# Optimization experiments

Measured on AMD Instinct MI355X. Metric: run time of the kernel, lower is better.

## Reference

```python
import jax, jax.numpy as jnp
import numpy as np

N, IN, H, OUT, E = 4096, 128, 128, 2, 131072


def _hgnn(x, G, W, b):
    # HGNNConv (Feng et al.): X' = G @ (X W + b), G dense normalized [N,N]
    return G @ (x @ W + b)


def _mha(xin, Wqkv, bqkv, Wo, bo, nh):
    # torch.nn.MultiheadAttention, input (L, B, E), self-attention, eval mode
    L, B, Emb = xin.shape
    hd = Emb // nh
    qkv = xin @ Wqkv.T + bqkv                       # [L,B,3E]
    q, k, v = jnp.split(qkv, 3, axis=-1)
    def sh(t):
        return t.reshape(L, B, nh, hd).transpose(1, 2, 0, 3)  # [B,nh,L,hd]
    q, k, v = sh(q), sh(k), sh(v)
    att = jax.nn.softmax(jnp.einsum('bnld,bnmd->bnlm', q, k) / jnp.sqrt(jnp.float32(hd)), axis=-1)
    o = jnp.einsum('bnlm,bnmd->bnld', att, v).transpose(2, 0, 1, 3).reshape(L, B, Emb)
    return o @ Wo.T + bo


def setup_inputs() -> dict:
    key = jax.random.key(0)
    ks = jax.random.split(key, 40)
    d = {}
    d['x'] = jax.random.normal(ks[0], (N, IN), jnp.float32)
    # dense normalized hypergraph propagation matrices (rand, scaled ~1/N so rows sum ~1)
    d['hg_1hop'] = jax.random.uniform(ks[1], (N, N), jnp.float32) * (2.0 / N)
    d['hg_3hop'] = jax.random.uniform(ks[2], (N, N), jnp.float32) * (2.0 / N)
    d['edge_indices'] = jax.random.randint(ks[3], (2, E), 0, N).astype(jnp.int32)
    d['new_idb'] = jax.random.permutation(ks[4], N).astype(jnp.int32)
    d['lam'] = jax.random.uniform(ks[5], (1,), jnp.float32)
    d['beta'] = jnp.asarray(0.3, jnp.float32)
    i = 6
    def w(shape, s):
        nonlocal i
        out = jax.random.normal(ks[i], shape, jnp.float32) * s
        i += 1
        return out
    sw = 1.0 / np.sqrt(H)
    d['W1'] = w((IN, H), 1.0 / np.sqrt(IN)); d['b1'] = w((H,), 0.01)
    for nm in ['W2', 'W3', 'W1h', 'W3h', 'W2m', 'W3m']:
        d[nm] = w((H, H), sw); d['b' + nm[1:]] = w((H,), 0.01)
    for tag in ['mix', 'fus']:
        d['Wqkv_' + tag] = w((3 * H, H), sw); d['bqkv_' + tag] = w((3 * H,), 0.01)
        d['Wo_' + tag] = w((H, H), sw); d['bo_' + tag] = w((H,), 0.01)
    d['Wc'] = w((2 * H, OUT), 1.0 / np.sqrt(2 * H)); d['bc'] = w((OUT,), 0.01)
    return d


def reference(x, hg_1hop, hg_3hop, edge_indices, new_idb, lam, beta,
              W1, b1, W2, b2, W3, b3, W1h, b1h, W3h, b3h, W2m, b2m, W3m, b3m,
              Wqkv_mix, bqkv_mix, Wo_mix, bo_mix,
              Wqkv_fus, bqkv_fus, Wo_fus, bo_fus, Wc, bc):
    # eval mode: dropout = identity
    h1 = jax.nn.relu(_hgnn(x, hg_1hop, W1, b1))
    h2 = jax.nn.relu(_hgnn(h1, hg_1hop, W2, b2) + h1)
    h3_c1 = jax.nn.relu(_hgnn(h2, hg_1hop, W3, b3) + h2)

    # shuffle_hypergraph: permute nodes of the dense incidence-derived matrix
    hg1_b = hg_1hop[new_idb][:, new_idb]
    hg3_b = hg_3hop[new_idb][:, new_idb]
    l = lam[0]
    # mixup_hidden: manifold mixup of propagated features with permuted graph/features
    h1_mix_1hop = l * _hgnn(h1, hg_1hop, W1h, b1h) + (1.0 - l) * _hgnn(h1[new_idb], hg1_b, W1h, b1h)
    h1_mix_3hop = l * _hgnn(h1, hg_3hop, W3h, b3h) + (1.0 - l) * _hgnn(h1[new_idb], hg3_b, W3h, b3h)

    h1_stack = jnp.stack([h1_mix_1hop, h1_mix_3hop], axis=0)     # [2,N,H]
    h1_mix = _mha(h1_stack, Wqkv_mix, bqkv_mix, Wo_mix, bo_mix, 2).mean(axis=0)
    h2_mix = jax.nn.relu(_hgnn(h1_mix, hg_1hop, W2m, b2m) + h1_mix)
    h3_c2 = jax.nn.relu(_hgnn(h2_mix, hg_1hop, W3m, b3m) + h2_mix) * beta

    h3_stack = jnp.stack([h3_c1, h3_c2], axis=0)                 # [2,N,H]
    h3 = _mha(h3_stack, Wqkv_fus, bqkv_fus, Wo_fus, bo_fus, 4).mean(axis=0)

    edge_emb = jnp.concatenate([h3[edge_indices[0]], h3[edge_indices[1]]], axis=1)  # [E,2H]
    edge_pred = edge_emb @ Wc + bc
    return edge_pred, h3
```

## Files before the change

kernel.cpp:

```cpp
#include <hip/hip_runtime.h>
#include <math.h>

typedef unsigned short u16;
typedef short s8v __attribute__((ext_vector_type(8)));
typedef float f4v __attribute__((ext_vector_type(4)));

__device__ inline float b2f(u16 u) {
    union { unsigned int i; float f; } v; v.i = ((unsigned int)u) << 16; return v.f;
}
__device__ inline u16 f2b(float f) {
    unsigned int x = __float_as_uint(f);
    return (u16)((x + 0x7fffu + ((x >> 16) & 1u)) >> 16);
}
__device__ inline float ldf(const void* p, size_t i, int f32) {
    return f32 ? ((const float*)p)[i] : b2f(((const u16*)p)[i]);
}
__device__ inline s8v load8(const void* p, size_t idx, int f32) {
    if (f32) {
        const float* f = (const float*)p + idx;
        float4 a = *(const float4*)(f);
        float4 b = *(const float4*)(f + 4);
        s8v r;
        r[0] = (short)f2b(a.x); r[1] = (short)f2b(a.y);
        r[2] = (short)f2b(a.z); r[3] = (short)f2b(a.w);
        r[4] = (short)f2b(b.x); r[5] = (short)f2b(b.y);
        r[6] = (short)f2b(b.z); r[7] = (short)f2b(b.w);
        return r;
    }
    return *(const s8v*)((const u16*)p + idx);
}

__global__ void detect_kernel(const u16* __restrict__ hg, int* __restrict__ flag) {
    int lane = threadIdx.x;
    bool ok = true;
    for (int i = 0; i < 32; ++i) {
        float v = b2f(hg[lane * 32 + i]);
        ok = ok && (fabsf(v) <= 1e-3f);
    }
    unsigned long long m = __ballot(ok);
    if (lane == 0) *flag = (m == ~0ull) ? 0 : 1;
}

__global__ __launch_bounds__(512) void big_gemm(const void* __restrict__ G,
                                                const u16* __restrict__ Zt,
                                                float* __restrict__ part,
                                                int kChunkLen,
                                                const int* __restrict__ dflag) {
    __shared__ u16 At[128 * 72];
    __shared__ u16 Bt[128 * 72];
    const int f32 = *dflag;
    const int tid = threadIdx.x;
    const int rowBase = blockIdx.x * 128;
    const int kChunk = blockIdx.y * kChunkLen;
    const int w = tid >> 6, lane = tid & 63;
    const int wm = w & 1, wn = w >> 1;
    const int l15 = lane & 15, quad = lane >> 4;
    const int nIter = kChunkLen >> 6;

    const int r0 = tid >> 3, kb0 = tid & 7;
    const int r1 = 64 + (tid >> 3), kb1 = tid & 7;

    f4v acc[4][2] = {};

    for (int it = 0; it < nIter; ++it) {
        const int kBase = kChunk + it * 64;
        s8v ga0 = load8(G, (size_t)(rowBase + r0) * 4096 + kBase + kb0 * 8, f32);
        s8v gb0 = *(const s8v*)(Zt + (size_t)r0 * 4096 + kBase + kb0 * 8);
        s8v ga1 = load8(G, (size_t)(rowBase + r1) * 4096 + kBase + kb1 * 8, f32);
        s8v gb1 = *(const s8v*)(Zt + (size_t)r1 * 4096 + kBase + kb1 * 8);
        __syncthreads();
        *(s8v*)(At + r0 * 72 + kb0 * 8) = ga0;
        *(s8v*)(Bt + r0 * 72 + kb0 * 8) = gb0;
        *(s8v*)(At + r1 * 72 + kb1 * 8) = ga1;
        *(s8v*)(Bt + r1 * 72 + kb1 * 8) = gb1;
        __syncthreads();
#pragma unroll
        for (int ks = 0; ks < 2; ++ks) {
            s8v a[4], b[2];
            const int kq = ks * 4 + quad;
#pragma unroll
            for (int mi = 0; mi < 4; ++mi)
                a[mi] = *(const s8v*)(At + (wm * 64 + mi * 16 + l15) * 72 + kq * 8);
#pragma unroll
            for (int ni = 0; ni < 2; ++ni)
                b[ni] = *(const s8v*)(Bt + (wn * 32 + ni * 16 + l15) * 72 + kq * 8);
#pragma unroll
            for (int mi = 0; mi < 4; ++mi)
#pragma unroll
                for (int ni = 0; ni < 2; ++ni)
                    acc[mi][ni] = __builtin_amdgcn_mfma_f32_16x16x32_bf16(
                        a[mi], b[ni], acc[mi][ni], 0, 0, 0);
        }
    }
    float* pbase = part + (size_t)blockIdx.y * 4096 * 128;
#pragma unroll
    for (int mi = 0; mi < 4; ++mi)
#pragma unroll
        for (int ni = 0; ni < 2; ++ni) {
            int row = rowBase + wm * 64 + mi * 16 + quad * 4;
            int col = wn * 32 + ni * 16 + l15;
#pragma unroll
            for (int r = 0; r < 4; ++r)
                pbase[(size_t)(row + r) * 128 + col] = acc[mi][ni][r];
        }
}

__global__ __launch_bounds__(256) void reduce_epi(const float* __restrict__ part,
                                                  const u16* __restrict__ res,
                                                  const void* __restrict__ betap,
                                                  u16* __restrict__ out, int mode,
                                                  int S, const int* __restrict__ dflag) {
    int i = (blockIdx.x * 256 + threadIdx.x) * 4;
    f4v t = {};
    for (int s = 0; s < S; ++s)
        t += *(const f4v*)(part + (size_t)s * 524288 + i);
    float bscale = (mode == 2) ? ldf(betap, 0, *dflag) : 1.0f;
    u16 o[4];
#pragma unroll
    for (int j = 0; j < 4; ++j) {
        float v = t[j];
        if (mode == 1 || mode == 2) v += b2f(res[i + j]);
        if (mode <= 2) v = fmaxf(v, 0.0f);
        if (mode == 2) v *= bscale;
        o[j] = f2b(v);
    }
    *(ushort4*)(out + i) = make_ushort4(o[0], o[1], o[2], o[3]);
}

__global__ __launch_bounds__(256) void feat_gemm(const void* __restrict__ A,
                                                 const void* __restrict__ W,
                                                 const void* __restrict__ bias,
                                                 void* __restrict__ out,
                                                 u16* __restrict__ mirror,
                                                 size_t outOfs,
                                                 int M, int NcTotal, int wLayout,
                                                 int outMode, int aRaw, int outRaw,
                                                 const int* __restrict__ dflag) {
    __shared__ char smem[52224];
    u16* Wt = (u16*)smem;
    u16* At = (u16*)(smem + 34816);
    u16* Tt = (u16*)smem;
    const int f32 = *dflag;
    const int aF32 = aRaw & f32;
    const int tid = threadIdx.x;
    const int rowBase = blockIdx.x * 64;
    const int colBase = blockIdx.y * 128;

    if (wLayout == 1) {
#pragma unroll
        for (int i = 0; i < 8; ++i) {
            int c = i * 256 + tid;
            int n = c >> 4, kb = c & 15;
            s8v v = load8(W, (size_t)(colBase + n) * 128 + kb * 8, f32);
            *(s8v*)(Wt + n * 136 + kb * 8) = v;
        }
    } else {
#pragma unroll
        for (int i = 0; i < 64; ++i) {
            int idx = i * 256 + tid;
            int k = idx >> 7, n = idx & 127;
            Wt[n * 136 + k] = f2b(ldf(W, (size_t)k * NcTotal + colBase + n, f32));
        }
    }
#pragma unroll
    for (int i = 0; i < 4; ++i) {
        int c = i * 256 + tid;
        int r = c >> 4, kb = c & 15;
        s8v v = load8(A, (size_t)(rowBase + r) * 128 + kb * 8, aF32);
        *(s8v*)(At + r * 136 + kb * 8) = v;
    }
    __syncthreads();

    const int w = tid >> 6, lane = tid & 63, l15 = lane & 15, quad = lane >> 4;
    f4v acc[8] = {};
#pragma unroll
    for (int ks = 0; ks < 4; ++ks) {
        int k = ks * 32 + quad * 8;
        s8v a = *(const s8v*)(At + (w * 16 + l15) * 136 + k);
#pragma unroll
        for (int ni = 0; ni < 8; ++ni) {
            s8v b = *(const s8v*)(Wt + (ni * 16 + l15) * 136 + k);
            acc[ni] = __builtin_amdgcn_mfma_f32_16x16x32_bf16(a, b, acc[ni], 0, 0, 0);
        }
    }

    if (outMode == 0) {
#pragma unroll
        for (int ni = 0; ni < 8; ++ni) {
            int n = colBase + ni * 16 + l15;
            float bv = ldf(bias, n, f32);
#pragma unroll
            for (int r = 0; r < 4; ++r) {
                int row = rowBase + w * 16 + quad * 4 + r;
                size_t idx = (size_t)row * NcTotal + n;
                float v = acc[ni][r] + bv;
                u16 vb = f2b(v);
                if (outRaw && f32) ((float*)out)[outOfs + idx] = v;
                else               ((u16*)out)[outOfs + idx] = vb;
                if (mirror) mirror[idx] = vb;
            }
        }
    } else {
        __syncthreads();
#pragma unroll
        for (int ni = 0; ni < 8; ++ni) {
            int n = ni * 16 + l15;
            float bv = ldf(bias, colBase + n, f32);
#pragma unroll
            for (int r = 0; r < 4; ++r)
                Tt[n * 72 + (w * 16 + quad * 4 + r)] = f2b(acc[ni][r] + bv);
        }
        __syncthreads();
#pragma unroll
        for (int i = 0; i < 4; ++i) {
            int c = i * 256 + tid;
            int h = c >> 3, nb = c & 7;
            s8v v = *(const s8v*)(Tt + h * 72 + nb * 8);
            *(s8v*)((u16*)out + (size_t)(colBase + h) * M + rowBase + nb * 8) = v;
        }
    }
}

__global__ __launch_bounds__(256) void mix_kernel(const u16* __restrict__ Ph1,
                                                  const u16* __restrict__ Ph3,
                                                  const int* __restrict__ perm,
                                                  const void* __restrict__ lamp,
                                                  u16* __restrict__ xin,
                                                  const int* __restrict__ dflag) {
    int i = blockIdx.x * 256 + threadIdx.x;
    int n = i >> 7, h = i & 127;
    float l = ldf(lamp, 0, *dflag);
    int pn = perm[n];
    float a = l * b2f(Ph1[i]) + (1.0f - l) * b2f(Ph1[(size_t)pn * 128 + h]);
    float b = l * b2f(Ph3[i]) + (1.0f - l) * b2f(Ph3[(size_t)pn * 128 + h]);
    xin[i] = f2b(a);
    xin[524288 + i] = f2b(b);
}

__global__ __launch_bounds__(256) void attn_kernel(const u16* __restrict__ qkv,
                                                   u16* __restrict__ obar, int nh) {
    int wid = threadIdx.x >> 6, lane = threadIdx.x & 63;
    int n = blockIdx.x * 4 + wid;
    const u16* r0 = qkv + (size_t)n * 384;
    const u16* r1 = qkv + (size_t)(4096 + n) * 384;
    int hd = 128 / nh;
    float scale = 1.0f / sqrtf((float)hd);
    float ov[2];
#pragma unroll
    for (int e = 0; e < 2; ++e) {
        int h = e * 64 + lane;
        float q0 = b2f(r0[h]),       q1 = b2f(r1[h]);
        float k0 = b2f(r0[128 + h]), k1 = b2f(r1[128 + h]);
        float v0 = b2f(r0[256 + h]), v1 = b2f(r1[256 + h]);
        float s00 = q0 * k0, s01 = q0 * k1, s10 = q1 * k0, s11 = q1 * k1;
        for (int off = hd >> 1; off; off >>= 1) {
            s00 += __shfl_xor(s00, off);
            s01 += __shfl_xor(s01, off);
            s10 += __shfl_xor(s10, off);
            s11 += __shfl_xor(s11, off);
        }
        s00 *= scale; s01 *= scale; s10 *= scale; s11 *= scale;
        float m0 = fmaxf(s00, s01), m1 = fmaxf(s10, s11);
        float e00 = expf(s00 - m0), e01 = expf(s01 - m0);
        float e10 = expf(s10 - m1), e11 = expf(s11 - m1);
        float a00 = e00 / (e00 + e01), a01 = e01 / (e00 + e01);
        float a10 = e10 / (e10 + e11), a11 = e11 / (e10 + e11);
        float o0 = a00 * v0 + a01 * v1;
        float o1 = a10 * v0 + a11 * v1;
        ov[e] = 0.5f * (o0 + o1);
    }
    obar[(size_t)n * 128 + lane] = f2b(ov[0]);
    obar[(size_t)n * 128 + 64 + lane] = f2b(ov[1]);
}

__global__ __launch_bounds__(256) void edge_kernel(const u16* __restrict__ h3,
                                                   const int* __restrict__ eidx,
                                                   const void* __restrict__ Wc,
                                                   const void* __restrict__ bc,
                                                   void* __restrict__ out,
                                                   const int* __restrict__ dflag) {
    __shared__ float w0[256], w1[256];
    const int f32 = *dflag;
    int t = threadIdx.x;
    w0[t] = ldf(Wc, (size_t)t * 2, f32);
    w1[t] = ldf(Wc, (size_t)t * 2 + 1, f32);
    __syncthreads();
    int e = blockIdx.x * 256 + t;
    float a0 = ldf(bc, 0, f32), a1 = ldf(bc, 1, f32);
#pragma unroll
    for (int p = 0; p < 2; ++p) {
        int node = eidx[p * 131072 + e];
        const s8v* row = (const s8v*)(h3 + (size_t)node * 128);
#pragma unroll
        for (int cch = 0; cch < 16; ++cch) {
            s8v d = row[cch];
#pragma unroll
            for (int j = 0; j < 8; ++j) {
                float f = b2f((u16)d[j]);
                int k = p * 128 + cch * 8 + j;
                a0 += f * w0[k];
                a1 += f * w1[k];
            }
        }
    }
    if (f32) {
        ((float*)out)[(size_t)e * 2] = a0;
        ((float*)out)[(size_t)e * 2 + 1] = a1;
    } else {
        ((u16*)out)[(size_t)e * 2] = f2b(a0);
        ((u16*)out)[(size_t)e * 2 + 1] = f2b(a1);
    }
}

extern "C" void kernel_launch(void* const* d_in, const int* in_sizes, int n_in,
                              void* d_out, int out_size, void* d_ws, size_t ws_size,
                              hipStream_t stream) {
    const void* x    = d_in[0];
    const void* G1   = d_in[1];
    const void* G3   = d_in[2];
    const int* eidx = (const int*)d_in[3];
    const int* perm = (const int*)d_in[4];
    const void* lam  = d_in[5];
    const void* beta = d_in[6];
    const void* W1 = d_in[7],  *b1 = d_in[8];
    const void* W2 = d_in[9],  *b2 = d_in[10];
    const void* W3 = d_in[11], *b3 = d_in[12];
    const void* W1h = d_in[13], *b1h = d_in[14];
    const void* W3h = d_in[15], *b3h = d_in[16];
    const void* W2m = d_in[17], *b2m = d_in[18];
    const void* W3m = d_in[19], *b3m = d_in[20];
    const void* Wqkv_mix = d_in[21], *bqkv_mix = d_in[22];
    const void* Wo_mix   = d_in[23], *bo_mix   = d_in[24];
    const void* Wqkv_fus = d_in[25], *bqkv_fus = d_in[26];
    const void* Wo_fus   = d_in[27], *bo_fus   = d_in[28];
    const void* Wc = d_in[29], *bc = d_in[30];

    const size_t MB = 1ull << 20;
    char* base = (char*)d_ws;
    u16* Zt    = (u16*)(base + 0 * MB);
    u16* h1    = (u16*)(base + 1 * MB);
    u16* h2    = (u16*)(base + 2 * MB);
    u16* h3c1  = (u16*)(base + 3 * MB);
    u16* h1mix = (u16*)(base + 4 * MB);
    u16* h2mix = (u16*)(base + 5 * MB);
    u16* h3c2  = (u16*)(base + 6 * MB);
    u16* Ph1   = (u16*)(base + 7 * MB);
    u16* Ph3   = (u16*)(base + 8 * MB);
    int* dflag = (int*)(base + 9 * MB);
    char* pool = base + 9 * MB + 65536;
    size_t poolBytes = (ws_size > 9 * MB + 65536) ? ws_size - 9 * MB - 65536 : 0;
    int S = (poolBytes >= 16 * MB) ? 8 : (poolBytes >= 8 * MB) ? 4
          : (poolBytes >= 4 * MB) ? 2 : 1;
    int kLen = 4096 / S;
    float* part = (float*)pool;
    u16* xin  = (u16*)pool;
    u16* qkv  = (u16*)(pool + 2 * MB);
    u16* obar = (u16*)pool;

    auto feat = [&](const void* A, const void* W, const void* b, void* o,
                    u16* mir, size_t ofs, int M, int Nc, int wl, int om,
                    int aRaw, int oRaw) {
        feat_gemm<<<dim3(M / 64, Nc / 128), 256, 0, stream>>>(
            A, W, b, o, mir, ofs, M, Nc, wl, om, aRaw, oRaw, dflag);
    };
    auto big = [&](const void* Gm) {
        big_gemm<<<dim3(32, S), 512, 0, stream>>>(Gm, Zt, part, kLen, dflag);
    };
    auto epi = [&](const u16* res, u16* o, int mode) {
        reduce_epi<<<512, 256, 0, stream>>>(part, res, beta, o, mode, S, dflag);
    };

    detect_kernel<<<1, 64, 0, stream>>>((const u16*)G1, dflag);

    feat(x, W1, b1, Zt, nullptr, 0, 4096, 128, 0, 1, 1, 0);  big(G1);  epi(nullptr, h1, 0);
    feat(h1, W2, b2, Zt, nullptr, 0, 4096, 128, 0, 1, 0, 0); big(G1);  epi(h1, h2, 1);
    feat(h1, W1h, b1h, Zt, nullptr, 0, 4096, 128, 0, 1, 0, 0); big(G1); epi(nullptr, Ph1, 3);
    feat(h1, W3h, b3h, Zt, nullptr, 0, 4096, 128, 0, 1, 0, 0); big(G3); epi(nullptr, Ph3, 3);
    feat(h2, W3, b3, Zt, nullptr, 0, 4096, 128, 0, 1, 0, 0); big(G1);  epi(h2, h3c1, 1);
    mix_kernel<<<2048, 256, 0, stream>>>(Ph1, Ph3, perm, lam, xin, dflag);
    feat(xin, Wqkv_mix, bqkv_mix, qkv, nullptr, 0, 8192, 384, 1, 0, 0, 0);
    attn_kernel<<<1024, 256, 0, stream>>>(qkv, obar, 2);
    feat(obar, Wo_mix, bo_mix, h1mix, nullptr, 0, 4096, 128, 1, 0, 0, 0);
    feat(h1mix, W2m, b2m, Zt, nullptr, 0, 4096, 128, 0, 1, 0, 0); big(G1); epi(h1mix, h2mix, 1);
    feat(h2mix, W3m, b3m, Zt, nullptr, 0, 4096, 128, 0, 1, 0, 0); big(G1); epi(h2mix, h3c2, 2);
    feat(h3c1, Wqkv_fus, bqkv_fus, qkv, nullptr, 0, 4096, 384, 1, 0, 0, 0);
    feat(h3c2, Wqkv_fus, bqkv_fus, qkv + (size_t)4096 * 384, nullptr, 0, 4096, 384, 1, 0, 0, 0);
    attn_kernel<<<1024, 256, 0, stream>>>(qkv, obar, 4);
    feat(obar, Wo_fus, bo_fus, d_out, Zt, (size_t)131072 * 2, 4096, 128, 1, 0, 0, 1);
    edge_kernel<<<512, 256, 0, stream>>>(Zt, eidx, Wc, bc, d_out, dflag);
}
```

Baseline: 643.4 us.

## Fuse whole forward into one cooperative persistent kernel with grid syncs

Replaces about thirty separate kernel launches with a single cooperative kernel of 256 blocks that runs every stage and separates them with grid.sync. It also converts G1 to bf16 once when the input is fp32, and runs independent feature and propagation GEMMs back to back within a phase (three big GEMMs into separate partial buffers), which removes launch gaps and some serialization. The cost is that the stages are tied to a fixed 256-block grid that may underuse the GPU, the kernel carries register and occupancy pressure, it needs 102 MB of workspace, and it falls back to the old path if the cooperative launch fails.

```diff
diff --git a/kernel.cpp b/kernel.cpp
--- a/kernel.cpp
+++ b/kernel.cpp
@@ -1,5 +1,8 @@
 #include <hip/hip_runtime.h>
+#include <hip/hip_cooperative_groups.h>
 #include <math.h>
+
+namespace cg = cooperative_groups;
 
 typedef unsigned short u16;
 typedef short s8v __attribute__((ext_vector_type(8)));
@@ -28,6 +31,318 @@
         return r;
     }
     return *(const s8v*)((const u16*)p + idx);
+}
+
+struct MP {
+    const void *x, *G1, *G3; const int *eidx, *perm; const void *lam, *beta;
+    const void *W1,*b1,*W2,*b2,*W3,*b3,*W1h,*b1h,*W3h,*b3h,*W2m,*b2m,*W3m,*b3m;
+    const void *Wqkv_mix,*bqkv_mix,*Wo_mix,*bo_mix,*Wqkv_fus,*bqkv_fus,*Wo_fus,*bo_fus,*Wc,*bc;
+    void* out;
+    u16 *G1b,*Zt0,*Zt1,*Zt2,*Zt3,*h1,*h2,*h3c1,*h1mix,*h2mix,*h3c2,*Ph1,*Ph3,*xin,*qkv,*obar,*mir;
+    float *part0,*part1,*part2;
+};
+
+__device__ void feat_stage(char* smemc, int bid, int tid, int f32,
+                           const void* A, int aF32,
+                           const void* W, const void* bias, int wLayout,
+                           int M, int Nc, int outMode, void* outp, u16* mir, int outF32) {
+    u16* Wt = (u16*)smemc;
+    u16* At = (u16*)(smemc + 34816);
+    const int w = tid >> 6, lane = tid & 63, l15 = lane & 15, quad = lane >> 4;
+    const int nSl = M >> 4;
+    for (int cb = 0; cb < Nc; cb += 128) {
+        __syncthreads();
+        if (wLayout == 1) {
+            for (int c = tid; c < 2048; c += 512) {
+                int n = c >> 4, kb = c & 15;
+                *(s8v*)(Wt + n * 136 + kb * 8) = load8(W, (size_t)(cb + n) * 128 + kb * 8, f32);
+            }
+        } else {
+            for (int idx = tid; idx < 16384; idx += 512) {
+                int k = idx >> 7, n = idx & 127;
+                Wt[n * 136 + k] = f2b(ldf(W, (size_t)k * Nc + cb + n, f32));
+            }
+        }
+        __syncthreads();
+        for (int sl = bid; sl < nSl; sl += 256) {
+            if (tid < 256) {
+                int r = tid >> 4, kb = tid & 15;
+                *(s8v*)(At + r * 136 + kb * 8) = load8(A, (size_t)(sl * 16 + r) * 128 + kb * 8, aF32);
+            }
+            __syncthreads();
+            f4v acc = {};
+#pragma unroll
+            for (int ks = 0; ks < 4; ++ks) {
+                s8v a = *(const s8v*)(At + l15 * 136 + ks * 32 + quad * 8);
+                s8v b = *(const s8v*)(Wt + (w * 16 + l15) * 136 + ks * 32 + quad * 8);
+                acc = __builtin_amdgcn_mfma_f32_16x16x32_bf16(a, b, acc, 0, 0, 0);
+            }
+            int col = cb + w * 16 + l15;
+            float bv = ldf(bias, col, f32);
+            if (outMode == 1) {
+                ushort4 o4;
+                o4.x = f2b(acc[0] + bv); o4.y = f2b(acc[1] + bv);
+                o4.z = f2b(acc[2] + bv); o4.w = f2b(acc[3] + bv);
+                *(ushort4*)((u16*)outp + (size_t)col * M + sl * 16 + quad * 4) = o4;
+            } else if (outMode == 0) {
+#pragma unroll
+                for (int r = 0; r < 4; ++r) {
+                    int row = sl * 16 + quad * 4 + r;
+                    ((u16*)outp)[(size_t)row * Nc + col] = f2b(acc[r] + bv);
+                }
+            } else {
+#pragma unroll
+                for (int r = 0; r < 4; ++r) {
+                    int row = sl * 16 + quad * 4 + r;
+                    float v = acc[r] + bv;
+                    u16 vb = f2b(v);
+                    mir[(size_t)row * 128 + col] = vb;
+                    if (outF32) ((float*)outp)[262144 + (size_t)row * 128 + col] = v;
+                    else        ((u16*)outp)[262144 + (size_t)row * 128 + col] = vb;
+                }
+            }
+            __syncthreads();
+        }
+    }
+}
+
+__device__ void big_stage(char* smemc, int tid, int id, const void* G, int gF32,
+                          const u16* Zt, float* part) {
+    u16* At = (u16*)smemc;
+    u16* Bt = (u16*)(smemc + 18432);
+    const int rowBase = (id & 31) * 128;
+    const int kChunk = (id >> 5) * 512;
+    const int w = tid >> 6, lane = tid & 63;
+    const int wm = w & 1, wn = w >> 1;
+    const int l15 = lane & 15, quad = lane >> 4;
+    const int r0 = tid >> 3, kb = tid & 7, r1 = 64 + (tid >> 3);
+    f4v acc[4][2] = {};
+    for (int it = 0; it < 8; ++it) {
+        const int kBase = kChunk + it * 64;
+        s8v ga0 = load8(G, (size_t)(rowBase + r0) * 4096 + kBase + kb * 8, gF32);
+        s8v gb0 = *(const s8v*)(Zt + (size_t)r0 * 4096 + kBase + kb * 8);
+        s8v ga1 = load8(G, (size_t)(rowBase + r1) * 4096 + kBase + kb * 8, gF32);
+        s8v gb1 = *(const s8v*)(Zt + (size_t)r1 * 4096 + kBase + kb * 8);
+        __syncthreads();
+        *(s8v*)(At + r0 * 72 + kb * 8) = ga0;
+        *(s8v*)(Bt + r0 * 72 + kb * 8) = gb0;
+        *(s8v*)(At + r1 * 72 + kb * 8) = ga1;
+        *(s8v*)(Bt + r1 * 72 + kb * 8) = gb1;
+        __syncthreads();
+#pragma unroll
+        for (int ks = 0; ks < 2; ++ks) {
+            s8v a[4], b[2];
+            const int kq = ks * 4 + quad;
+#pragma unroll
+            for (int mi = 0; mi < 4; ++mi)
+                a[mi] = *(const s8v*)(At + (wm * 64 + mi * 16 + l15) * 72 + kq * 8);
+#pragma unroll
+            for (int ni = 0; ni < 2; ++ni)
+                b[ni] = *(const s8v*)(Bt + (wn * 32 + ni * 16 + l15) * 72 + kq * 8);
+#pragma unroll
+            for (int mi = 0; mi < 4; ++mi)
+#pragma unroll
+                for (int ni = 0; ni < 2; ++ni)
+                    acc[mi][ni] = __builtin_amdgcn_mfma_f32_16x16x32_bf16(
+                        a[mi], b[ni], acc[mi][ni], 0, 0, 0);
+        }
+    }
+    float* pbase = part + (size_t)(id >> 5) * 524288;
+#pragma unroll
+    for (int mi = 0; mi < 4; ++mi)
+#pragma unroll
+        for (int ni = 0; ni < 2; ++ni) {
+            int row = rowBase + wm * 64 + mi * 16 + quad * 4;
+            int col = wn * 32 + ni * 16 + l15;
+#pragma unroll
+            for (int r = 0; r < 4; ++r)
+                pbase[(size_t)(row + r) * 128 + col] = acc[mi][ni][r];
+        }
+}
+
+__device__ void epi_one(int gid, const float* part, const u16* res, u16* outb,
+                        int mode, float bscale) {
+    int i = gid * 4;
+    f4v t = {};
+#pragma unroll
+    for (int s = 0; s < 8; ++s)
+        t += *(const f4v*)(part + (size_t)s * 524288 + i);
+    u16 o[4];
+#pragma unroll
+    for (int j = 0; j < 4; ++j) {
+        float v = t[j];
+        if (mode == 1 || mode == 2) v += b2f(res[i + j]);
+        if (mode <= 2) v = fmaxf(v, 0.0f);
+        if (mode == 2) v *= bscale;
+        o[j] = f2b(v);
+    }
+    *(ushort4*)(outb + i) = make_ushort4(o[0], o[1], o[2], o[3]);
+}
+
+__device__ void mix_stage(int gid, const u16* Ph1, const u16* Ph3,
+                          const int* perm, float l, u16* xin) {
+    for (int i = gid; i < 524288; i += 131072) {
+        int n = i >> 7, h = i & 127;
+        int pn = perm[n];
+        float a = l * b2f(Ph1[i]) + (1.0f - l) * b2f(Ph1[(size_t)pn * 128 + h]);
+        float b = l * b2f(Ph3[i]) + (1.0f - l) * b2f(Ph3[(size_t)pn * 128 + h]);
+        xin[i] = f2b(a);
+        xin[524288 + i] = f2b(b);
+    }
+}
+
+__device__ void attn_stage(int bid, int tid, const u16* qkv, u16* obar, int nh) {
+    int w = tid >> 6, lane = tid & 63;
+    int hd = 128 / nh;
+    float scale = 1.0f / sqrtf((float)hd);
+    for (int n = bid * 8 + w; n < 4096; n += 2048) {
+        const u16* r0 = qkv + (size_t)n * 384;
+        const u16* r1 = qkv + (size_t)(4096 + n) * 384;
+        float ov[2];
+#pragma unroll
+        for (int e = 0; e < 2; ++e) {
+            int h = e * 64 + lane;
+            float q0 = b2f(r0[h]),       q1 = b2f(r1[h]);
+            float k0 = b2f(r0[128 + h]), k1 = b2f(r1[128 + h]);
+            float v0 = b2f(r0[256 + h]), v1 = b2f(r1[256 + h]);
+            float s00 = q0 * k0, s01 = q0 * k1, s10 = q1 * k0, s11 = q1 * k1;
+            for (int off = hd >> 1; off; off >>= 1) {
+                s00 += __shfl_xor(s00, off);
+                s01 += __shfl_xor(s01, off);
+                s10 += __shfl_xor(s10, off);
+                s11 += __shfl_xor(s11, off);
+            }
+            s00 *= scale; s01 *= scale; s10 *= scale; s11 *= scale;
+            float m0 = fmaxf(s00, s01), m1 = fmaxf(s10, s11);
+            float e00 = expf(s00 - m0), e01 = expf(s01 - m0);
+            float e10 = expf(s10 - m1), e11 = expf(s11 - m1);
+            float a00 = e00 / (e00 + e01), a01 = e01 / (e00 + e01);
+            float a10 = e10 / (e10 + e11), a11 = e11 / (e10 + e11);
+            ov[e] = 0.5f * ((a00 * v0 + a01 * v1) + (a10 * v0 + a11 * v1));
+        }
+        obar[(size_t)n * 128 + lane] = f2b(ov[0]);
+        obar[(size_t)n * 128 + 64 + lane] = f2b(ov[1]);
+    }
+}
+
+__device__ void edge_stage(char* smemc, int bid, int tid, int f32, const u16* h3,
+                           const int* eidx, const void* Wc, const void* bc, void* out) {
+    float* w0 = (float*)smemc;
+    float* w1 = (float*)(smemc + 1024);
+    __syncthreads();
+    if (tid < 256) {
+        w0[tid] = ldf(Wc, (size_t)tid * 2, f32);
+        w1[tid] = ldf(Wc, (size_t)tid * 2 + 1, f32);
+    }
+    __syncthreads();
+    int e = bid * 512 + tid;
+    float a0 = ldf(bc, 0, f32), a1 = ldf(bc, 1, f32);
+#pragma unroll
+    for (int p = 0; p < 2; ++p) {
+        int node = eidx[p * 131072 + e];
+        const s8v* row = (const s8v*)(h3 + (size_t)node * 128);
+#pragma unroll
+        for (int cch = 0; cch < 16; ++cch) {
+            s8v d = row[cch];
+#pragma unroll
+            for (int j = 0; j < 8; ++j) {
+                float f = b2f((u16)d[j]);
+                int k = p * 128 + cch * 8 + j;
+                a0 += f * w0[k];
+                a1 += f * w1[k];
+            }
+        }
+    }
+    if (f32) {
+        ((float*)out)[(size_t)e * 2] = a0;
+        ((float*)out)[(size_t)e * 2 + 1] = a1;
+    } else {
+        ((u16*)out)[(size_t)e * 2] = f2b(a0);
+        ((u16*)out)[(size_t)e * 2 + 1] = f2b(a1);
+    }
+}
+
+__global__ __launch_bounds__(512) void mega(MP P) {
+    __shared__ char smem[40960];
+    __shared__ int s_flag;
+    cg::grid_group grid = cg::this_grid();
+    const int tid = threadIdx.x, bid = blockIdx.x;
+    const int gid = bid * 512 + tid;
+
+    if (tid == 0) s_flag = 0;
+    __syncthreads();
+    {
+        int bad = 0;
+        for (int i = tid; i < 2048; i += 512) {
+            float v = b2f(((const u16*)P.G1)[i]);
+            if (!(fabsf(v) <= 1e-3f)) bad = 1;
+        }
+        if (bad) atomicOr(&s_flag, 1);
+    }
+    __syncthreads();
+    const int f32 = s_flag;
+
+    if (f32) {
+        for (size_t c = (size_t)gid; c < 2097152; c += 131072)
+            *(s8v*)(P.G1b + c * 8) = load8(P.G1, c * 8, 1);
+    }
+    const u16* G1u = f32 ? P.G1b : (const u16*)P.G1;
+    grid.sync();
+
+    feat_stage(smem, bid, tid, f32, P.x, f32, P.W1, P.b1, 0, 4096, 128, 1, P.Zt0, 0, 0);
+    grid.sync();
+    big_stage(smem, tid, bid, G1u, 0, P.Zt0, P.part0);
+    grid.sync();
+    epi_one(gid, P.part0, 0, P.h1, 0, 1.0f);
+    grid.sync();
+
+    feat_stage(smem, bid, tid, f32, P.h1, 0, P.W2,  P.b2,  0, 4096, 128, 1, P.Zt1, 0, 0);
+    feat_stage(smem, bid, tid, f32, P.h1, 0, P.W1h, P.b1h, 0, 4096, 128, 1, P.Zt2, 0, 0);
+    feat_stage(smem, bid, tid, f32, P.h1, 0, P.W3h, P.b3h, 0, 4096, 128, 1, P.Zt3, 0, 0);
+    grid.sync();
+    big_stage(smem, tid, bid, G1u, 0, P.Zt1, P.part0);
+    big_stage(smem, tid, bid, G1u, 0, P.Zt2, P.part1);
+    big_stage(smem, tid, bid, P.G3, f32, P.Zt3, P.part2);
+    grid.sync();
+    epi_one(gid, P.part0, P.h1, P.h2, 1, 1.0f);
+    epi_one(gid, P.part1, 0, P.Ph1, 3, 1.0f);
+    epi_one(gid, P.part2, 0, P.Ph3, 3, 1.0f);
+    grid.sync();
+
+    mix_stage(gid, P.Ph1, P.Ph3, P.perm, ldf(P.lam, 0, f32), P.xin);
+    feat_stage(smem, bid, tid, f32, P.h2, 0, P.W3, P.b3, 0, 4096, 128, 1, P.Zt0, 0, 0);
+    grid.sync();
+    big_stage(smem, tid, bid, G1u, 0, P.Zt0, P.part0);
+    feat_stage(smem, bid, tid, f32, P.xin, 0, P.Wqkv_mix, P.bqkv_mix, 1, 8192, 384, 0, P.qkv, 0, 0);
+    grid.sync();
+    epi_one(gid, P.part0, P.h2, P.h3c1, 1, 1.0f);
+    attn_stage(bid, tid, P.qkv, P.obar, 2);
+    grid.sync();
+    feat_stage(smem, bid, tid, f32, P.obar, 0, P.Wo_mix, P.bo_mix, 1, 4096, 128, 0, P.h1mix, 0, 0);
+    grid.sync();
+
+    feat_stage(smem, bid, tid, f32, P.h1mix, 0, P.W2m, P.b2m, 0, 4096, 128, 1, P.Zt0, 0, 0);
+    grid.sync();
+    big_stage(smem, tid, bid, G1u, 0, P.Zt0, P.part0);
+    grid.sync();
+    epi_one(gid, P.part0, P.h1mix, P.h2mix, 1, 1.0f);
+    grid.sync();
+    feat_stage(smem, bid, tid, f32, P.h2mix, 0, P.W3m, P.b3m, 0, 4096, 128, 1, P.Zt0, 0, 0);
+    grid.sync();
+    big_stage(smem, tid, bid, G1u, 0, P.Zt0, P.part0);
+    grid.sync();
+    epi_one(gid, P.part0, P.h2mix, P.h3c2, 2, ldf(P.beta, 0, f32));
+    grid.sync();
+
+    feat_stage(smem, bid, tid, f32, P.h3c1, 0, P.Wqkv_fus, P.bqkv_fus, 1, 4096, 384, 0, P.qkv, 0, 0);
+    feat_stage(smem, bid, tid, f32, P.h3c2, 0, P.Wqkv_fus, P.bqkv_fus, 1, 4096, 384, 0,
+               P.qkv + (size_t)4096 * 384, 0, 0);
+    grid.sync();
+    attn_stage(bid, tid, P.qkv, P.obar, 4);
+    grid.sync();
+    feat_stage(smem, bid, tid, f32, P.obar, 0, P.Wo_fus, P.bo_fus, 1, 4096, 128, 2, P.out, P.mir, f32);
+    grid.sync();
+    edge_stage(smem, bid, tid, f32, P.mir, P.eidx, P.Wc, P.bc, P.out);
 }
 
 __global__ void detect_kernel(const u16* __restrict__ hg, int* __restrict__ flag) {
@@ -56,12 +371,9 @@
     const int wm = w & 1, wn = w >> 1;
     const int l15 = lane & 15, quad = lane >> 4;
     const int nIter = kChunkLen >> 6;
-
     const int r0 = tid >> 3, kb0 = tid & 7;
     const int r1 = 64 + (tid >> 3), kb1 = tid & 7;
-
     f4v acc[4][2] = {};
-
     for (int it = 0; it < nIter; ++it) {
         const int kBase = kChunk + it * 64;
         s8v ga0 = load8(G, (size_t)(rowBase + r0) * 4096 + kBase + kb0 * 8, f32);
@@ -136,23 +448,21 @@
                                                  int M, int NcTotal, int wLayout,
                                                  int outMode, int aRaw, int outRaw,
                                                  const int* __restrict__ dflag) {
-    __shared__ char smem[52224];
-    u16* Wt = (u16*)smem;
-    u16* At = (u16*)(smem + 34816);
-    u16* Tt = (u16*)smem;
+    __shared__ char smemf[52224];
+    u16* Wt = (u16*)smemf;
+    u16* At = (u16*)(smemf + 34816);
+    u16* Tt = (u16*)smemf;
     const int f32 = *dflag;
     const int aF32 = aRaw & f32;
     const int tid = threadIdx.x;
     const int rowBase = blockIdx.x * 64;
     const int colBase = blockIdx.y * 128;
-
     if (wLayout == 1) {
 #pragma unroll
         for (int i = 0; i < 8; ++i) {
             int c = i * 256 + tid;
             int n = c >> 4, kb = c & 15;
-            s8v v = load8(W, (size_t)(colBase + n) * 128 + kb * 8, f32);
-            *(s8v*)(Wt + n * 136 + kb * 8) = v;
+            *(s8v*)(Wt + n * 136 + kb * 8) = load8(W, (size_t)(colBase + n) * 128 + kb * 8, f32);
         }
     } else {
 #pragma unroll
@@ -166,11 +476,9 @@
     for (int i = 0; i < 4; ++i) {
         int c = i * 256 + tid;
         int r = c >> 4, kb = c & 15;
-        s8v v = load8(A, (size_t)(rowBase + r) * 128 + kb * 8, aF32);
-        *(s8v*)(At + r * 136 + kb * 8) = v;
+        *(s8v*)(At + r * 136 + kb * 8) = load8(A, (size_t)(rowBase + r) * 128 + kb * 8, aF32);
     }
     __syncthreads();
-
     const int w = tid >> 6, lane = tid & 63, l15 = lane & 15, quad = lane >> 4;
     f4v acc[8] = {};
 #pragma unroll
@@ -183,7 +491,6 @@
             acc[ni] = __builtin_amdgcn_mfma_f32_16x16x32_bf16(a, b, acc[ni], 0, 0, 0);
         }
     }
-
     if (outMode == 0) {
 #pragma unroll
         for (int ni = 0; ni < 8; ++ni) {
@@ -265,9 +572,7 @@
         float e10 = expf(s10 - m1), e11 = expf(s11 - m1);
         float a00 = e00 / (e00 + e01), a01 = e01 / (e00 + e01);
         float a10 = e10 / (e10 + e11), a11 = e11 / (e10 + e11);
-        float o0 = a00 * v0 + a01 * v1;
-        float o1 = a10 * v0 + a11 * v1;
-        ov[e] = 0.5f * (o0 + o1);
+        ov[e] = 0.5f * ((a00 * v0 + a01 * v1) + (a10 * v0 + a11 * v1));
     }
     obar[(size_t)n * 128 + lane] = f2b(ov[0]);
     obar[(size_t)n * 128 + 64 + lane] = f2b(ov[1]);
@@ -315,28 +620,56 @@
 extern "C" void kernel_launch(void* const* d_in, const int* in_sizes, int n_in,
                               void* d_out, int out_size, void* d_ws, size_t ws_size,
                               hipStream_t stream) {
-    const void* x    = d_in[0];
-    const void* G1   = d_in[1];
-    const void* G3   = d_in[2];
-    const int* eidx = (const int*)d_in[3];
-    const int* perm = (const int*)d_in[4];
-    const void* lam  = d_in[5];
-    const void* beta = d_in[6];
-    const void* W1 = d_in[7],  *b1 = d_in[8];
-    const void* W2 = d_in[9],  *b2 = d_in[10];
-    const void* W3 = d_in[11], *b3 = d_in[12];
-    const void* W1h = d_in[13], *b1h = d_in[14];
-    const void* W3h = d_in[15], *b3h = d_in[16];
-    const void* W2m = d_in[17], *b2m = d_in[18];
-    const void* W3m = d_in[19], *b3m = d_in[20];
-    const void* Wqkv_mix = d_in[21], *bqkv_mix = d_in[22];
-    const void* Wo_mix   = d_in[23], *bo_mix   = d_in[24];
-    const void* Wqkv_fus = d_in[25], *bqkv_fus = d_in[26];
-    const void* Wo_fus   = d_in[27], *bo_fus   = d_in[28];
-    const void* Wc = d_in[29], *bc = d_in[30];
-
     const size_t MB = 1ull << 20;
     char* base = (char*)d_ws;
+
+    MP P;
+    P.x = d_in[0]; P.G1 = d_in[1]; P.G3 = d_in[2];
+    P.eidx = (const int*)d_in[3]; P.perm = (const int*)d_in[4];
+    P.lam = d_in[5]; P.beta = d_in[6];
+    P.W1 = d_in[7];  P.b1 = d_in[8];
+    P.W2 = d_in[9];  P.b2 = d_in[10];
+    P.W3 = d_in[11]; P.b3 = d_in[12];
+    P.W1h = d_in[13]; P.b1h = d_in[14];
+    P.W3h = d_in[15]; P.b3h = d_in[16];
+    P.W2m = d_in[17]; P.b2m = d_in[18];
+    P.W3m = d_in[19]; P.b3m = d_in[20];
+    P.Wqkv_mix = d_in[21]; P.bqkv_mix = d_in[22];
+    P.Wo_mix = d_in[23];   P.bo_mix = d_in[24];
+    P.Wqkv_fus = d_in[25]; P.bqkv_fus = d_in[26];
+    P.Wo_fus = d_in[27];   P.bo_fus = d_in[28];
+    P.Wc = d_in[29]; P.bc = d_in[30];
+    P.out = d_out;
+    P.G1b   = (u16*)(base);
+    P.part0 = (float*)(base + 32 * MB);
+    P.part1 = (float*)(base + 48 * MB);
+    P.part2 = (float*)(base + 64 * MB);
+    P.Zt0   = (u16*)(base + 80 * MB);
+    P.Zt1   = (u16*)(base + 81 * MB);
+    P.Zt2   = (u16*)(base + 82 * MB);
+    P.Zt3   = (u16*)(base + 83 * MB);
+    P.h1    = (u16*)(base + 84 * MB);
+    P.h2    = (u16*)(base + 85 * MB);
+    P.h3c1  = (u16*)(base + 86 * MB);
+    P.h1mix = (u16*)(base + 87 * MB);
+    P.h2mix = (u16*)(base + 88 * MB);
+    P.h3c2  = (u16*)(base + 89 * MB);
+    P.Ph1   = (u16*)(base + 90 * MB);
+    P.Ph3   = (u16*)(base + 91 * MB);
+    P.xin   = (u16*)(base + 92 * MB);
+    P.qkv   = (u16*)(base + 94 * MB);
+    P.obar  = (u16*)(base + 100 * MB);
+    P.mir   = (u16*)(base + 101 * MB);
+
+    hipError_t err = hipErrorUnknown;
+    if (ws_size >= 102 * MB) {
+        void* args[] = { &P };
+        err = hipLaunchCooperativeKernel((const void*)mega, dim3(256), dim3(512),
+                                         args, 0, stream);
+    }
+    if (err == hipSuccess) return;
+    (void)hipGetLastError();
+
     u16* Zt    = (u16*)(base + 0 * MB);
     u16* h1    = (u16*)(base + 1 * MB);
     u16* h2    = (u16*)(base + 2 * MB);
@@ -367,25 +700,24 @@
         big_gemm<<<dim3(32, S), 512, 0, stream>>>(Gm, Zt, part, kLen, dflag);
     };
     auto epi = [&](const u16* res, u16* o, int mode) {
-        reduce_epi<<<512, 256, 0, stream>>>(part, res, beta, o, mode, S, dflag);
+        reduce_epi<<<512, 256, 0, stream>>>(part, res, P.beta, o, mode, S, dflag);
     };
 
-    detect_kernel<<<1, 64, 0, stream>>>((const u16*)G1, dflag);
-
-    feat(x, W1, b1, Zt, nullptr, 0, 4096, 128, 0, 1, 1, 0);  big(G1);  epi(nullptr, h1, 0);
-    feat(h1, W2, b2, Zt, nullptr, 0, 4096, 128, 0, 1, 0, 0); big(G1);  epi(h1, h2, 1);
-    feat(h1, W1h, b1h, Zt, nullptr, 0, 4096, 128, 0, 1, 0, 0); big(G1); epi(nullptr, Ph1, 3);
-    feat(h1, W3h, b3h, Zt, nullptr, 0, 4096, 128, 0, 1, 0, 0); big(G3); epi(nullptr, Ph3, 3);
-    feat(h2, W3, b3, Zt, nullptr, 0, 4096, 128, 0, 1, 0, 0); big(G1);  epi(h2, h3c1, 1);
-    mix_kernel<<<2048, 256, 0, stream>>>(Ph1, Ph3, perm, lam, xin, dflag);
-    feat(xin, Wqkv_mix, bqkv_mix, qkv, nullptr, 0, 8192, 384, 1, 0, 0, 0);
+    detect_kernel<<<1, 64, 0, stream>>>((const u16*)P.G1, dflag);
+    feat(P.x, P.W1, P.b1, Zt, nullptr, 0, 4096, 128, 0, 1, 1, 0);  big(P.G1);  epi(nullptr, h1, 0);
+    feat(h1, P.W2, P.b2, Zt, nullptr, 0, 4096, 128, 0, 1, 0, 0); big(P.G1);  epi(h1, h2, 1);
+    feat(h1, P.W1h, P.b1h, Zt, nullptr, 0, 4096, 128, 0, 1, 0, 0); big(P.G1); epi(nullptr, Ph1, 3);
+    feat(h1, P.W3h, P.b3h, Zt, nullptr, 0, 4096, 128, 0, 1, 0, 0); big(P.G3); epi(nullptr, Ph3, 3);
+    feat(h2, P.W3, P.b3, Zt, nullptr, 0, 4096, 128, 0, 1, 0, 0); big(P.G1);  epi(h2, h3c1, 1);
+    mix_kernel<<<2048, 256, 0, stream>>>(Ph1, Ph3, P.perm, P.lam, xin, dflag);
+    feat(xin, P.Wqkv_mix, P.bqkv_mix, qkv, nullptr, 0, 8192, 384, 1, 0, 0, 0);
     attn_kernel<<<1024, 256, 0, stream>>>(qkv, obar, 2);
-    feat(obar, Wo_mix, bo_mix, h1mix, nullptr, 0, 4096, 128, 1, 0, 0, 0);
-    feat(h1mix, W2m, b2m, Zt, nullptr, 0, 4096, 128, 0, 1, 0, 0); big(G1); epi(h1mix, h2mix, 1);
-    feat(h2mix, W3m, b3m, Zt, nullptr, 0, 4096, 128, 0, 1, 0, 0); big(G1); epi(h2mix, h3c2, 2);
-    feat(h3c1, Wqkv_fus, bqkv_fus, qkv, nullptr, 0, 4096, 384, 1, 0, 0, 0);
-    feat(h3c2, Wqkv_fus, bqkv_fus, qkv + (size_t)4096 * 384, nullptr, 0, 4096, 384, 1, 0, 0, 0);
+    feat(obar, P.Wo_mix, P.bo_mix, h1mix, nullptr, 0, 4096, 128, 1, 0, 0, 0);
+    feat(h1mix, P.W2m, P.b2m, Zt, nullptr, 0, 4096, 128, 0, 1, 0, 0); big(P.G1); epi(h1mix, h2mix, 1);
+    feat(h2mix, P.W3m, P.b3m, Zt, nullptr, 0, 4096, 128, 0, 1, 0, 0); big(P.G1); epi(h2mix, h3c2, 2);
+    feat(h3c1, P.Wqkv_fus, P.bqkv_fus, qkv, nullptr, 0, 4096, 384, 1, 0, 0, 0);
+    feat(h3c2, P.Wqkv_fus, P.bqkv_fus, qkv + (size_t)4096 * 384, nullptr, 0, 4096, 384, 1, 0, 0, 0);
     attn_kernel<<<1024, 256, 0, stream>>>(qkv, obar, 4);
-    feat(obar, Wo_fus, bo_fus, d_out, Zt, (size_t)131072 * 2, 4096, 128, 1, 0, 0, 1);
-    edge_kernel<<<512, 256, 0, stream>>>(Zt, eidx, Wc, bc, d_out, dflag);
-}
+    feat(obar, P.Wo_fus, P.bo_fus, d_out, Zt, (size_t)131072 * 2, 4096, 128, 1, 0, 0, 1);
+    edge_kernel<<<512, 256, 0, stream>>>(Zt, P.eidx, P.Wc, P.bc, d_out, dflag);
+}
```

Measured after the change: 1.096 ms. 1.7x slower.
